# Optimization experiments

Hardware: AMD Instinct MI355X
Metric: run time of the kernel (lower is better)

Reference implementation:

```python
import jax, jax.numpy as jnp
import numpy as np

IOU_THRESH = 0.5
NEG_POS_RATIO = 3
VAR0, VAR1 = 0.1, 0.2  # BoxCoder variances


def box_iou(a, b):
    # a: [G,4] xyxy, b: [P,4] xyxy -> [G,P]
    lt = jnp.maximum(a[:, None, :2], b[None, :, :2])
    rb = jnp.minimum(a[:, None, 2:], b[None, :, 2:])
    wh = jnp.clip(rb - lt, 0.0)
    inter = wh[..., 0] * wh[..., 1]
    area_a = (a[:, 2] - a[:, 0]) * (a[:, 3] - a[:, 1])
    area_b = (b[:, 2] - b[:, 0]) * (b[:, 3] - b[:, 1])
    return inter / (area_a[:, None] + area_b[None, :] - inter)


def xywha_to_xyxy(p):
    c, wh = p[:, :2], p[:, 2:]
    return jnp.concatenate([c - wh * 0.5, c + wh * 0.5], axis=-1)


def assign_targets(gt_boxes, gt_labels, priors_xyxy):
    # gt_boxes [G,4], gt_labels [G], priors_xyxy [P,4]
    iou = box_iou(gt_boxes, priors_xyxy)            # [G,P]
    matched_vals = iou.max(axis=0)                  # [P]
    matches = iou.argmax(axis=0)                    # [P]
    best_prior = iou.argmax(axis=1)                 # [G] best prior per target
    G = gt_boxes.shape[0]
    matches = matches.at[best_prior].set(jnp.arange(G))
    matched_vals = matched_vals.at[best_prior].set(2.0)
    labels = jnp.where(matched_vals < IOU_THRESH, 0, gt_labels[matches])  # [P]
    boxes = gt_boxes[matches]                       # [P,4]
    return boxes, labels


def encode(boxes_xyxy, priors_xywha):
    # SSD center-form encoding with variances
    ctr = (boxes_xyxy[:, :2] + boxes_xyxy[:, 2:]) * 0.5
    wh = boxes_xyxy[:, 2:] - boxes_xyxy[:, :2]
    g_c = (ctr - priors_xywha[:, :2]) / (VAR0 * priors_xywha[:, 2:])
    g_wh = jnp.log(wh / priors_xywha[:, 2:]) / VAR1
    return jnp.concatenate([g_c, g_wh], axis=-1)


def hard_negative_mask(bg_loss, labels):
    # bg_loss [B,P]: -log_softmax(logits)[...,0]; keep all positives and
    # top-(ratio*num_pos) hardest negatives per image.
    pos = labels > 0
    num_neg = pos.sum(axis=1, keepdims=True) * NEG_POS_RATIO
    loss = jnp.where(pos, -jnp.inf, bg_loss)
    order = jnp.argsort(-loss, axis=1)
    rank = jnp.argsort(order, axis=1)
    return pos | (rank < num_neg)


def reference(priors, class_logits, box_regression, gt_boxes, gt_labels):
    priors_xyxy = xywha_to_xyxy(priors)
    boxes, labels = jax.vmap(assign_targets, in_axes=(0, 0, None))(
        gt_boxes, gt_labels, priors_xyxy)            # [B,P,4], [B,P]
    regression_targets = jax.vmap(encode, in_axes=(0, None))(boxes, priors)

    logp = jax.nn.log_softmax(class_logits, axis=-1)  # [B,P,C]
    bg_loss = jax.lax.stop_gradient(-logp[..., 0])
    mask = hard_negative_mask(bg_loss, labels)        # [B,P] bool

    # masked cross-entropy, reduction='sum'
    ce = -jnp.take_along_axis(logp, labels[..., None], axis=-1)[..., 0]
    loss_classifier = jnp.sum(jnp.where(mask, ce, 0.0))

    # masked smooth-L1 (beta=1), reduction='sum' over positives
    pos = labels > 0
    d = jnp.abs(box_regression - regression_targets)
    sl1 = jnp.where(d < 1.0, 0.5 * d * d, d - 0.5)
    loss_box_reg = jnp.sum(jnp.where(pos[..., None], sl1, 0.0))

    num_pos = jnp.sum(pos).astype(class_logits.dtype)
    return loss_box_reg / num_pos, loss_classifier / num_pos


def setup_inputs() -> dict:
    key = jax.random.key(0)
    ks = jax.random.split(key, 8)
    B, P, C, G = 64, 8732, 81, 16
    # priors: xywha in [0,1] with small positive wh
    p_c = jax.random.uniform(ks[0], (P, 2), jnp.float32, 0.05, 0.95)
    p_wh = jax.random.uniform(ks[1], (P, 2), jnp.float32, 0.02, 0.25)
    priors = jnp.concatenate([p_c, p_wh], axis=-1)
    class_logits = jax.random.normal(ks[2], (B, P, C), jnp.float32)
    box_regression = jax.random.normal(ks[3], (B, P, 4), jnp.float32)
    # gt boxes: valid xyxy in [0,1] with positive size
    g_c = jax.random.uniform(ks[4], (B, G, 2), jnp.float32, 0.2, 0.8)
    g_wh = jax.random.uniform(ks[5], (B, G, 2), jnp.float32, 0.05, 0.3)
    gt_boxes = jnp.concatenate([g_c - g_wh * 0.5, g_c + g_wh * 0.5], axis=-1)
    gt_labels = jax.random.randint(ks[6], (B, G), 1, C, jnp.int32)
    return {"priors": priors, "class_logits": class_logits,
            "box_regression": box_regression, "gt_boxes": gt_boxes,
            "gt_labels": gt_labels}
```

## Files before the change

### kernel.cpp

```cpp
#include <hip/hip_runtime.h>
#include <cfloat>

#define GT 16
#define NCLS 81
#define TPB 256
#define MAXP 8732
#define TROWS 64
#define TF4 (TROWS*NCLS/4)

__device__ __forceinline__ float smoothl1(float d){
  float a = fabsf(d);
  return a < 1.0f ? 0.5f*a*a : a - 0.5f;
}

__global__ __launch_bounds__(TPB) void assign1(
    const float* __restrict__ priors,
    const float* __restrict__ gt_boxes,
    long long* __restrict__ best,
    float* __restrict__ mvv,
    unsigned char* __restrict__ mmatch,
    float* __restrict__ ce_pos, float* __restrict__ sl1_sum,
    int* __restrict__ num_pos, float* __restrict__ out,
    int P)
{
  const int b = blockIdx.x >> 3, chunk = blockIdx.x & 7;
  const int CH = (P + 7) >> 3;
  const int p0 = chunk*CH, p1 = min(p0 + CH, P);
  const int tid = threadIdx.x, wave = tid >> 6, lane = tid & 63;
  if (chunk == 0 && tid == 0){ ce_pos[b] = 0.0f; sl1_sum[b] = 0.0f; num_pos[b] = 0; }
  if (blockIdx.x == 0 && tid < 2) out[tid] = 0.0f;
  __shared__ float gx0[GT], gy0[GT], gx1[GT], gy1[GT], ga[GT];
  __shared__ float redv[4*GT]; __shared__ int redi[4*GT];
  if (tid < GT){
    const float4 gb = ((const float4*)gt_boxes)[b*GT + tid];
    gx0[tid]=gb.x; gy0[tid]=gb.y; gx1[tid]=gb.z; gy1[tid]=gb.w;
    ga[tid] = (gb.z-gb.x)*(gb.w-gb.y);
  }
  __syncthreads();
  float bv[GT]; int bi[GT];
  #pragma unroll
  for (int g=0; g<GT; ++g){ bv[g] = -1.0f; bi[g] = 0x7fffffff; }
  for (int p = p0 + tid; p < p1; p += TPB){
    const float4 pr = ((const float4*)priors)[p];
    const float px0 = pr.x - pr.z*0.5f, py0 = pr.y - pr.w*0.5f;
    const float px1 = pr.x + pr.z*0.5f, py1 = pr.y + pr.w*0.5f;
    const float pa = (px1-px0)*(py1-py0);
    float mv = -1.0f; int mi = 0;
    #pragma unroll
    for (int g=0; g<GT; ++g){
      const float w = fmaxf(fminf(gx1[g],px1) - fmaxf(gx0[g],px0), 0.0f);
      const float h = fmaxf(fminf(gy1[g],py1) - fmaxf(gy0[g],py0), 0.0f);
      const float inter = w*h;
      const float iou = inter / (ga[g] + pa - inter);
      if (iou > mv){ mv = iou; mi = g; }
      if (iou > bv[g]){ bv[g] = iou; bi[g] = p; }
    }
    mvv[(long long)b*P + p] = mv;
    mmatch[(long long)b*P + p] = (unsigned char)mi;
  }
  #pragma unroll
  for (int g=0; g<GT; ++g){
    float v = bv[g]; int i = bi[g];
    for (int off=32; off>0; off>>=1){
      const float ov = __shfl_down(v, off);
      const int   oi = __shfl_down(i, off);
      if (ov > v || (ov == v && oi < i)){ v = ov; i = oi; }
    }
    if (lane == 0){ redv[wave*GT+g] = v; redi[wave*GT+g] = i; }
  }
  __syncthreads();
  if (tid < GT){
    float v = redv[tid]; int i = redi[tid];
    for (int w=1; w<4; ++w){
      const float ov = redv[w*GT+tid]; const int oi = redi[w*GT+tid];
      if (ov > v || (ov == v && oi < i)){ v = ov; i = oi; }
    }
    const long long pk =
      ((long long)(unsigned long long)__float_as_uint(v) << 32)
      | (long long)(0xFFFFFFFFu - (unsigned)i);
    atomicMax(&best[b*GT + tid], pk);
  }
}

__global__ __launch_bounds__(TPB) void assign2(
    const float* __restrict__ priors,
    const float* __restrict__ gt_boxes,
    const int*   __restrict__ gt_labels,
    const float* __restrict__ box_reg,
    const long long* __restrict__ best,
    const float* __restrict__ mvv,
    const unsigned char* __restrict__ mmatch,
    int*   __restrict__ labels_out,
    float* __restrict__ sl1_sum,
    int*   __restrict__ num_pos,
    int P)
{
  const int b = blockIdx.x >> 3, chunk = blockIdx.x & 7;
  const int CH = (P + 7) >> 3;
  const int p0 = chunk*CH, p1 = min(p0 + CH, P);
  const int tid = threadIdx.x, wave = tid >> 6, lane = tid & 63;
  __shared__ float gx0[GT], gy0[GT], gx1[GT], gy1[GT];
  __shared__ int glab[GT], bp[GT];
  __shared__ float rs[4]; __shared__ int rc[4];
  if (tid < GT){
    const float4 gb = ((const float4*)gt_boxes)[b*GT + tid];
    gx0[tid]=gb.x; gy0[tid]=gb.y; gx1[tid]=gb.z; gy1[tid]=gb.w;
    glab[tid] = gt_labels[b*GT + tid];
    bp[tid] = (int)(0xFFFFFFFFu - (unsigned)((unsigned long long)best[b*GT + tid] & 0xFFFFFFFFull));
  }
  __syncthreads();
  float sl1 = 0.0f; int cnt = 0;
  for (int p = p0 + tid; p < p1; p += TPB){
    float mv = mvv[(long long)b*P + p];
    int g = mmatch[(long long)b*P + p];
    #pragma unroll
    for (int g2=0; g2<GT; ++g2) if (bp[g2] == p){ mv = 2.0f; g = g2; }
    int lab = 0;
    if (mv >= 0.5f){
      lab = glab[g]; cnt++;
      const float4 pr = ((const float4*)priors)[p];
      const float ctrx = (gx0[g]+gx1[g])*0.5f, ctry = (gy0[g]+gy1[g])*0.5f;
      const float wx = gx1[g]-gx0[g], wy = gy1[g]-gy0[g];
      const float tx = (ctrx - pr.x) / (0.1f*pr.z);
      const float ty = (ctry - pr.y) / (0.1f*pr.w);
      const float tw = __logf(wx/pr.z) / 0.2f;
      const float th = __logf(wy/pr.w) / 0.2f;
      const float4 br = ((const float4*)box_reg)[(long long)b*P + p];
      sl1 += smoothl1(br.x - tx) + smoothl1(br.y - ty)
           + smoothl1(br.z - tw) + smoothl1(br.w - th);
    }
    labels_out[(long long)b*P + p] = lab;
  }
  float v = sl1; int c = cnt;
  for (int off=32; off>0; off>>=1){ v += __shfl_down(v, off); c += __shfl_down(c, off); }
  if (lane == 0){ rs[wave] = v; rc[wave] = c; }
  __syncthreads();
  if (tid == 0){
    atomicAdd(&sl1_sum[b], rs[0]+rs[1]+rs[2]+rs[3]);
    atomicAdd(&num_pos[b], rc[0]+rc[1]+rc[2]+rc[3]);
  }
}

__global__ __launch_bounds__(TPB) void lse_pipe(
    const float* __restrict__ logits,
    const int*   __restrict__ labels,
    float* __restrict__ bg,
    float* __restrict__ ce_pos,
    int P, int NT)
{
  __shared__ float s[TROWS*NCLS];
  const int tid = threadIdx.x;
  const int G = gridDim.x;
  int t = blockIdx.x;
  if (t >= NT) return;
  const int rl = tid >> 2, q = tid & 3;
  const int c0 = q ? (1+20*q) : 0;
  const int c1 = 21 + 20*q;

  float4 r0,r1,r2,r3,r4,r5; int labc;
  {
    const float4* src = (const float4*)logits + (long long)t*TF4;
    r0 = src[tid]; r1 = src[tid+256]; r2 = src[tid+512];
    r3 = src[tid+768]; r4 = src[tid+1024];
    if (tid < TF4-1280) r5 = src[tid+1280];
    labc = labels[(long long)t*TROWS + rl];
  }
  for (; t < NT; t += G){
    __syncthreads();
    float4* sd = (float4*)s;
    sd[tid] = r0; sd[tid+256] = r1; sd[tid+512] = r2;
    sd[tid+768] = r3; sd[tid+1024] = r4;
    if (tid < TF4-1280) sd[tid+1280] = r5;
    __syncthreads();
    const int lab = labc;
    const int tn = t + G;
    if (tn < NT){
      const float4* src = (const float4*)logits + (long long)tn*TF4;
      r0 = src[tid]; r1 = src[tid+256]; r2 = src[tid+512];
      r3 = src[tid+768]; r4 = src[tid+1024];
      if (tid < TF4-1280) r5 = src[tid+1280];
      labc = labels[(long long)tn*TROWS + rl];
    }
    const float* x = s + rl*NCLS;
    float sum = 0.0f;
    for (int c = c0; c < c1; ++c) sum += __expf(x[c]);
    sum += __shfl_xor(sum, 1);
    sum += __shfl_xor(sum, 2);
    if (q == 0){
      const long long row = (long long)t*TROWS + rl;
      const float lse = __logf(sum);
      float bgv;
      if (lab > 0){
        const int b = (int)(row / P);
        const float xl = x[lab];
        atomicAdd(&ce_pos[b], lse - xl);
        bgv = 0.0f;
      } else {
        bgv = fmaxf(lse - x[0], 0.0f);
      }
      bg[row] = bgv;
    }
  }
}

__global__ __launch_bounds__(TPB) void topk_kernel(
    const float* __restrict__ bg,
    const int*   __restrict__ num_pos,
    const float* __restrict__ sl1_sum,
    const float* __restrict__ ce_pos,
    float* __restrict__ out,
    int P, int B)
{
  const int b = blockIdx.x;
  const int tid = threadIdx.x;
  const int wave = tid >> 6, lane = tid & 63;
  const int rep = tid & 15;
  __shared__ float sv[MAXP];
  __shared__ unsigned cntR[16][256];
  __shared__ float    sumR[16][256];
  __shared__ unsigned s_wc[4];
  __shared__ float    s_wf[4];
  __shared__ unsigned s_prefix;
  __shared__ int s_krem, s_chosen, s_newk;
  __shared__ float s_total, s_addf;

  {
    const float4* srcp = (const float4*)(bg + (long long)b * P);
    float4* dst = (float4*)sv;
    for (int j = tid; j < P/4; j += TPB) dst[j] = srcp[j];
  }
  if (tid == 0){
    const int k = 3*num_pos[b];
    s_krem = k < P ? k : P-1;
    s_total = 0.0f; s_prefix = 0u;
  }
  __syncthreads();

  for (int level=0; level<4; ++level){
    const int shift = 24 - 8*level;
    for (int i = tid; i < 4096; i += TPB){
      ((unsigned*)cntR)[i] = 0u; ((float*)sumR)[i] = 0.0f;
    }
    __syncthreads();
    const unsigned pref = s_prefix;
    const int k = s_krem;
    for (int p = tid; p < P; p += TPB){
      const float f = sv[p];
      const unsigned key = __float_as_uint(f);
      const bool ok = (level == 0) || ((key >> (shift+8)) == pref);
      if (ok){
        const unsigned bin = (key >> shift) & 255u;
        atomicAdd(&cntR[rep][bin], 1u);
        atomicAdd(&sumR[rep][bin], f);
      }
    }
    __syncthreads();
    const int rb = 255 - tid;
    unsigned c = 0; float fs = 0.0f;
    #pragma unroll
    for (int r=0; r<16; ++r){ c += cntR[r][rb]; fs += sumR[r][rb]; }
    unsigned cv = c; float fv = fs;
    #pragma unroll
    for (int off=1; off<64; off<<=1){
      const unsigned oc = __shfl_up(cv, off);
      const float    of = __shfl_up(fv, off);
      if (lane >= off){ cv += oc; fv += of; }
    }
    if (lane == 63){ s_wc[wave] = cv; s_wf[wave] = fv; }
    __syncthreads();
    unsigned addc = 0; float addf = 0.0f;
    for (int w=0; w<4; ++w) if (w < wave){ addc += s_wc[w]; addf += s_wf[w]; }
    const unsigned S  = cv - c + addc;
    const float    Sf = fv - fs + addf;
    if ((int)S <= k && k < (int)(S + c)){
      s_chosen = rb; s_newk = k - (int)S; s_addf = Sf;
    }
    __syncthreads();
    if (tid == 0){
      s_total += s_addf;
      s_krem = s_newk;
      s_prefix = (pref << 8) | (unsigned)s_chosen;
    }
    __syncthreads();
  }
  if (tid < 64){
    float n = 0.0f;
    for (int i = tid; i < B; i += 64) n += (float)num_pos[i];
    for (int off=32; off>0; off>>=1) n += __shfl_down(n, off);
    if (tid == 0){
      const float N = n;
      const float cls = s_total + (float)s_krem * __uint_as_float(s_prefix);
      atomicAdd(&out[0], sl1_sum[b] / N);
      atomicAdd(&out[1], (ce_pos[b] + cls) / N);
    }
  }
}

extern "C" void kernel_launch(void* const* d_in, const int* in_sizes, int n_in,
                              void* d_out, int out_size, void* d_ws, size_t ws_size,
                              hipStream_t stream) {
  const float* priors = (const float*)d_in[0];
  const float* logits = (const float*)d_in[1];
  const float* boxreg = (const float*)d_in[2];
  const float* gtb    = (const float*)d_in[3];
  const int*   gtl    = (const int*)d_in[4];
  const int P = in_sizes[0] / 4;
  const int B = in_sizes[4] / GT;
  const long long BP = (long long)B * P;

  char* ws = (char*)d_ws;
  int*   labels = (int*)ws;
  float* bgmv   = (float*)(ws + BP*4);
  unsigned char* mmatch = (unsigned char*)(ws + BP*8);
  char* tail = ws + BP*9;
  long long* best = (long long*)tail;
  float* sl1_s  = (float*)(tail + (long long)B*GT*8);
  int*   npos   = (int*)  (tail + (long long)B*GT*8 + 256);
  float* ce_pos = (float*)(tail + (long long)B*GT*8 + 512);

  assign1<<<B*8, TPB, 0, stream>>>(priors, gtb, best, bgmv, mmatch,
                                   ce_pos, sl1_s, npos, (float*)d_out, P);
  assign2<<<B*8, TPB, 0, stream>>>(priors, gtb, gtl, boxreg, best, bgmv, mmatch,
                                   labels, sl1_s, npos, P);
  const int NT = (int)(BP / TROWS);
  const int G = 1792;
  lse_pipe<<<G, TPB, 0, stream>>>(logits, labels, bgmv, ce_pos, P, NT);
  topk_kernel<<<B, TPB, 0, stream>>>(bgmv, npos, sl1_s, ce_pos, (float*)d_out, P, B);
}
```

Baseline: 365.7 us.

## Use per-wave LDS tiles in LSE pass and count-only radix select

```diff
diff --git a/kernel.cpp b/kernel.cpp
--- a/kernel.cpp
+++ b/kernel.cpp
@@ -6,6 +6,7 @@
 #define TPB 256
 #define MAXP 8732
 #define TROWS 64
+#define WF4 324
 #define TF4 (TROWS*NCLS/4)
 
 __device__ __forceinline__ float smoothl1(float d){
@@ -150,48 +151,47 @@
 {
   __shared__ float s[TROWS*NCLS];
   const int tid = threadIdx.x;
+  const int wave = tid >> 6, lane = tid & 63;
+  const int rl = lane >> 2, q = lane & 3;
+  const int c0 = q ? (1+20*q) : 0;
+  const int c1 = 21 + 20*q;
   const int G = gridDim.x;
   int t = blockIdx.x;
   if (t >= NT) return;
-  const int rl = tid >> 2, q = tid & 3;
-  const int c0 = q ? (1+20*q) : 0;
-  const int c1 = 21 + 20*q;
-
-  float4 r0,r1,r2,r3,r4,r5; int labc;
+
+  float4 r0,r1,r2,r3,r4,r5; int labc = 0;
   {
-    const float4* src = (const float4*)logits + (long long)t*TF4;
-    r0 = src[tid]; r1 = src[tid+256]; r2 = src[tid+512];
-    r3 = src[tid+768]; r4 = src[tid+1024];
-    if (tid < TF4-1280) r5 = src[tid+1280];
-    labc = labels[(long long)t*TROWS + rl];
-  }
+    const float4* src = (const float4*)logits + (long long)t*TF4 + wave*WF4;
+    r0 = src[lane]; r1 = src[lane+64]; r2 = src[lane+128];
+    r3 = src[lane+192]; r4 = src[lane+256];
+    if (lane < 4) r5 = src[lane+320];
+    if (q == 0) labc = labels[t*TROWS + wave*16 + rl];
+  }
+  float4* sd = (float4*)(s) + wave*WF4;
+  const float* x = s + wave*(WF4*4) + rl*NCLS;
   for (; t < NT; t += G){
-    __syncthreads();
-    float4* sd = (float4*)s;
-    sd[tid] = r0; sd[tid+256] = r1; sd[tid+512] = r2;
-    sd[tid+768] = r3; sd[tid+1024] = r4;
-    if (tid < TF4-1280) sd[tid+1280] = r5;
-    __syncthreads();
+    sd[lane] = r0; sd[lane+64] = r1; sd[lane+128] = r2;
+    sd[lane+192] = r3; sd[lane+256] = r4;
+    if (lane < 4) sd[lane+320] = r5;
     const int lab = labc;
     const int tn = t + G;
     if (tn < NT){
-      const float4* src = (const float4*)logits + (long long)tn*TF4;
-      r0 = src[tid]; r1 = src[tid+256]; r2 = src[tid+512];
-      r3 = src[tid+768]; r4 = src[tid+1024];
-      if (tid < TF4-1280) r5 = src[tid+1280];
-      labc = labels[(long long)tn*TROWS + rl];
-    }
-    const float* x = s + rl*NCLS;
+      const float4* src = (const float4*)logits + (long long)tn*TF4 + wave*WF4;
+      r0 = src[lane]; r1 = src[lane+64]; r2 = src[lane+128];
+      r3 = src[lane+192]; r4 = src[lane+256];
+      if (lane < 4) r5 = src[lane+320];
+      if (q == 0) labc = labels[tn*TROWS + wave*16 + rl];
+    }
     float sum = 0.0f;
     for (int c = c0; c < c1; ++c) sum += __expf(x[c]);
     sum += __shfl_xor(sum, 1);
     sum += __shfl_xor(sum, 2);
     if (q == 0){
-      const long long row = (long long)t*TROWS + rl;
+      const int row = t*TROWS + wave*16 + rl;
       const float lse = __logf(sum);
       float bgv;
       if (lab > 0){
-        const int b = (int)(row / P);
+        const int b = row / P;
         const float xl = x[lab];
         atomicAdd(&ce_pos[b], lse - xl);
         bgv = 0.0f;
@@ -216,13 +216,11 @@
   const int wave = tid >> 6, lane = tid & 63;
   const int rep = tid & 15;
   __shared__ float sv[MAXP];
-  __shared__ unsigned cntR[16][256];
-  __shared__ float    sumR[16][256];
+  __shared__ unsigned cntR[16][257];
   __shared__ unsigned s_wc[4];
   __shared__ float    s_wf[4];
   __shared__ unsigned s_prefix;
   __shared__ int s_krem, s_chosen, s_newk;
-  __shared__ float s_total, s_addf;
 
   {
     const float4* srcp = (const float4*)(bg + (long long)b * P);
@@ -232,64 +230,72 @@
   if (tid == 0){
     const int k = 3*num_pos[b];
     s_krem = k < P ? k : P-1;
-    s_total = 0.0f; s_prefix = 0u;
+    s_prefix = 0u;
   }
   __syncthreads();
 
   for (int level=0; level<4; ++level){
     const int shift = 24 - 8*level;
-    for (int i = tid; i < 4096; i += TPB){
-      ((unsigned*)cntR)[i] = 0u; ((float*)sumR)[i] = 0.0f;
-    }
+    for (int i = tid; i < 16*257; i += TPB) ((unsigned*)cntR)[i] = 0u;
     __syncthreads();
     const unsigned pref = s_prefix;
     const int k = s_krem;
-    for (int p = tid; p < P; p += TPB){
-      const float f = sv[p];
-      const unsigned key = __float_as_uint(f);
-      const bool ok = (level == 0) || ((key >> (shift+8)) == pref);
-      if (ok){
-        const unsigned bin = (key >> shift) & 255u;
-        atomicAdd(&cntR[rep][bin], 1u);
-        atomicAdd(&sumR[rep][bin], f);
+    for (int j = tid; j < P/4; j += TPB){
+      const float4 f4 = ((const float4*)sv)[j];
+      #pragma unroll
+      for (int e=0; e<4; ++e){
+        const unsigned key = __float_as_uint((&f4.x)[e]);
+        const bool ok = (level == 0) || ((key >> (shift+8)) == pref);
+        if (ok) atomicAdd(&cntR[rep][(key >> shift) & 255u], 1u);
       }
     }
     __syncthreads();
     const int rb = 255 - tid;
-    unsigned c = 0; float fs = 0.0f;
-    #pragma unroll
-    for (int r=0; r<16; ++r){ c += cntR[r][rb]; fs += sumR[r][rb]; }
-    unsigned cv = c; float fv = fs;
+    unsigned c = 0;
+    #pragma unroll
+    for (int r=0; r<16; ++r) c += cntR[r][rb];
+    unsigned cv = c;
     #pragma unroll
     for (int off=1; off<64; off<<=1){
       const unsigned oc = __shfl_up(cv, off);
-      const float    of = __shfl_up(fv, off);
-      if (lane >= off){ cv += oc; fv += of; }
-    }
-    if (lane == 63){ s_wc[wave] = cv; s_wf[wave] = fv; }
-    __syncthreads();
-    unsigned addc = 0; float addf = 0.0f;
-    for (int w=0; w<4; ++w) if (w < wave){ addc += s_wc[w]; addf += s_wf[w]; }
-    const unsigned S  = cv - c + addc;
-    const float    Sf = fv - fs + addf;
+      if (lane >= off) cv += oc;
+    }
+    if (lane == 63) s_wc[wave] = cv;
+    __syncthreads();
+    unsigned addc = 0;
+    for (int w=0; w<4; ++w) if (w < wave) addc += s_wc[w];
+    const unsigned S = cv - c + addc;
     if ((int)S <= k && k < (int)(S + c)){
-      s_chosen = rb; s_newk = k - (int)S; s_addf = Sf;
+      s_chosen = rb; s_newk = k - (int)S;
     }
     __syncthreads();
     if (tid == 0){
-      s_total += s_addf;
       s_krem = s_newk;
       s_prefix = (pref << 8) | (unsigned)s_chosen;
     }
     __syncthreads();
   }
+  const unsigned T = s_prefix;
+  float acc = 0.0f;
+  for (int j = tid; j < P/4; j += TPB){
+    const float4 f4 = ((const float4*)sv)[j];
+    #pragma unroll
+    for (int e=0; e<4; ++e){
+      const float f = (&f4.x)[e];
+      if (__float_as_uint(f) > T) acc += f;
+    }
+  }
+  for (int off=32; off>0; off>>=1) acc += __shfl_down(acc, off);
+  if (lane == 0) s_wf[wave] = acc;
+  __syncthreads();
   if (tid < 64){
     float n = 0.0f;
     for (int i = tid; i < B; i += 64) n += (float)num_pos[i];
     for (int off=32; off>0; off>>=1) n += __shfl_down(n, off);
     if (tid == 0){
       const float N = n;
-      const float cls = s_total + (float)s_krem * __uint_as_float(s_prefix);
+      const float cls = s_wf[0]+s_wf[1]+s_wf[2]+s_wf[3]
+                      + (float)s_krem * __uint_as_float(T);
       atomicAdd(&out[0], sl1_sum[b] / N);
       atomicAdd(&out[1], (ce_pos[b] + cls) / N);
     }
```

Result: faster. 340.6 us (-6.9%).
